# Optimization experiments

Measured on AMD Instinct MI355X. Metric: run time of the kernel, lower is better.

## Reference

```python
import jax, jax.numpy as jnp
import numpy as np

DIM = 64          # out_channels == mamba d_model
D_INNER = 2 * DIM # mamba expand=2
D_STATE = 16
DT_RANK = 4       # ceil(DIM/16)
D_CONV = 4


def setup_inputs() -> dict:
    key = jax.random.key(0)
    ks = jax.random.split(key, 12)
    B, Cin, H, W = 4, 32, 192, 192
    x = jax.random.normal(ks[0], (B, Cin, H, W), jnp.float32)
    conv_w = jax.random.normal(ks[1], (DIM, Cin, 4, 4), jnp.float32) * (1.0 / np.sqrt(Cin * 16))
    conv_b = jnp.zeros((DIM,), jnp.float32)
    ln_g = jnp.ones((DIM,), jnp.float32)
    ln_b = jnp.zeros((DIM,), jnp.float32)
    in_proj_w = jax.random.normal(ks[2], (2 * D_INNER, DIM), jnp.float32) * (1.0 / np.sqrt(DIM))
    conv1d_w = jax.random.normal(ks[3], (D_INNER, 1, D_CONV), jnp.float32) * (1.0 / np.sqrt(D_CONV))
    conv1d_b = jnp.zeros((D_INNER,), jnp.float32)
    x_proj_w = jax.random.normal(ks[4], (DT_RANK + 2 * D_STATE, D_INNER), jnp.float32) * (1.0 / np.sqrt(D_INNER))
    dt_proj_w = jax.random.normal(ks[5], (D_INNER, DT_RANK), jnp.float32) * (DT_RANK ** -0.5)
    dt_proj_b = jnp.log(jnp.expm1(jnp.exp(jax.random.uniform(ks[6], (D_INNER,), jnp.float32,
                jnp.log(1e-3), jnp.log(1e-1)))))  # softplus-inverse of dt in [1e-3,1e-1]
    A_log = jnp.log(jnp.tile(jnp.arange(1, D_STATE + 1, dtype=jnp.float32)[None, :], (D_INNER, 1)))
    D = jnp.ones((D_INNER,), jnp.float32)
    out_proj_w = jax.random.normal(ks[7], (DIM, D_INNER), jnp.float32) * (1.0 / np.sqrt(D_INNER))
    return {"x": x, "conv_w": conv_w, "conv_b": conv_b, "ln_g": ln_g, "ln_b": ln_b,
            "in_proj_w": in_proj_w, "conv1d_w": conv1d_w, "conv1d_b": conv1d_b,
            "x_proj_w": x_proj_w, "dt_proj_w": dt_proj_w, "dt_proj_b": dt_proj_b,
            "A_log": A_log, "D": D, "out_proj_w": out_proj_w}


def _mamba(seq, in_proj_w, conv1d_w, conv1d_b, x_proj_w, dt_proj_w, dt_proj_b, A_log, D, out_proj_w):
    # seq: (B, L, DIM)
    Bb, L, _ = seq.shape
    xz = seq @ in_proj_w.T                          # (B, L, 2*d_inner)
    xm, z = jnp.split(xz, 2, axis=-1)
    # causal depthwise conv1d along L
    xc = jnp.transpose(xm, (0, 2, 1))               # (B, d_inner, L)
    xc = jnp.pad(xc, ((0, 0), (0, 0), (D_CONV - 1, 0)))
    xc = jax.lax.conv_general_dilated(xc, conv1d_w, (1,), 'VALID',
                                      dimension_numbers=('NCH', 'OIH', 'NCH'),
                                      feature_group_count=D_INNER)
    xm = jax.nn.silu(jnp.transpose(xc + conv1d_b[None, :, None], (0, 2, 1)))  # (B, L, d_inner)
    x_dbl = xm @ x_proj_w.T                         # (B, L, dt_rank + 2*d_state)
    dt, Bs, Cs = jnp.split(x_dbl, [DT_RANK, DT_RANK + D_STATE], axis=-1)
    dt = jax.nn.softplus(dt @ dt_proj_w.T + dt_proj_b)  # (B, L, d_inner)
    A = -jnp.exp(A_log)                             # (d_inner, d_state)
    dA = jnp.exp(dt[..., None] * A)                 # (B, L, d_inner, d_state)
    dBx = (dt * xm)[..., None] * Bs[:, :, None, :]  # (B, L, d_inner, d_state)

    def step(h, t):
        dA_t, dBx_t, C_t = t
        h = dA_t * h + dBx_t                        # (B, d_inner, d_state)
        return h, jnp.einsum('bds,bs->bd', h, C_t)

    h0 = jnp.zeros((Bb, D_INNER, D_STATE), seq.dtype)
    _, ys = jax.lax.scan(step, h0, (jnp.swapaxes(dA, 0, 1), jnp.swapaxes(dBx, 0, 1), jnp.swapaxes(Cs, 0, 1)))
    y = jnp.swapaxes(ys, 0, 1) + xm * D             # (B, L, d_inner)
    y = y * jax.nn.silu(z)
    return y @ out_proj_w.T                          # (B, L, DIM)


def reference(x, conv_w, conv_b, ln_g, ln_b, in_proj_w, conv1d_w, conv1d_b,
              x_proj_w, dt_proj_w, dt_proj_b, A_log, D, out_proj_w):
    # ReflectionPad2d(1) + Conv2d(k=4, s=2)
    xp = jnp.pad(x, ((0, 0), (0, 0), (1, 1), (1, 1)), mode='reflect')
    xc = jax.lax.conv_general_dilated(xp, conv_w, (2, 2), 'VALID',
                                      dimension_numbers=('NCHW', 'OIHW', 'NCHW'))
    xc = xc + conv_b[None, :, None, None]           # (B, DIM, H/2, W/2)
    Bb, C, H, W = xc.shape
    seq = jnp.transpose(xc.reshape(Bb, C, H * W), (0, 2, 1))  # (B, L, C)
    mu = seq.mean(-1, keepdims=True)
    var = seq.var(-1, keepdims=True)
    nrm = (seq - mu) * jax.lax.rsqrt(var + 1e-5) * ln_g + ln_b
    out = _mamba(nrm, in_proj_w, conv1d_w, conv1d_b, x_proj_w, dt_proj_w,
                 dt_proj_b, A_log, D, out_proj_w) + seq        # SingleMambaBlock residual
    out = jnp.transpose(out, (0, 2, 1)).reshape(Bb, C, H, W)
    return out + xc                                 # outer residual in Mamba_block.forward
```

## Files before the change

### kernel.cpp

```cpp
#include <hip/hip_runtime.h>
#include <hip/hip_bf16.h>

#define B_   4
#define CIN  32
#define HIN  192
#define WIN  192
#define HO   96
#define WO   96
#define L_   9216
#define C_   64
#define DI   128
#define DS   16
#define NC   256
#define CL   36

typedef unsigned short u16t;
typedef unsigned int   u32t;
typedef short s16x8 __attribute__((ext_vector_type(8)));
typedef float f32x4 __attribute__((ext_vector_type(4)));

__device__ __forceinline__ u16t f2b(float f) {
    u32t u = __float_as_uint(f);
    return (u16t)((u + 0x7fffu + ((u >> 16) & 1u)) >> 16);
}
__device__ __forceinline__ float b2f(u16t h) { return __uint_as_float(((u32t)h) << 16); }
__device__ __forceinline__ void split2(float v, u16t& hi, u16t& lo) {
    hi = f2b(v);
    lo = f2b(v - b2f(hi));
}

#define MFMA16(a, b, c) __builtin_amdgcn_mfma_f32_16x16x32_bf16((a), (b), (c), 0, 0, 0)

__global__ __launch_bounds__(256) void k0_prep(
    const float* __restrict__ ipw, const float* __restrict__ xpw,
    const float* __restrict__ dtw, const float* __restrict__ opw,
    const float* __restrict__ cw,
    u16t* __restrict__ W2p, u16t* __restrict__ Wcp, u16t* __restrict__ W6p,
    u16t* __restrict__ Bp)
{
    int i = blockIdx.x * 256 + threadIdx.x;
    if (i < 32768) {
        int e = i & 7, ln = (i >> 3) & 63, hl = (i >> 9) & 1;
        int nt = (i >> 10) & 15, kt = i >> 14;
        int n = nt * 16 + (ln & 15), k = kt * 32 + (ln >> 4) * 8 + e;
        u16t hi, lo; split2(ipw[n * 64 + k], hi, lo);
        W2p[i] = hl ? lo : hi;
    } else if (i < 32768 + 40960) {
        int j = i - 32768;
        int e = j & 7, ln = (j >> 3) & 63, hl = (j >> 9) & 1;
        int r = j >> 10; int nt = r % 10, kt = r / 10;
        int n = nt * 16 + (ln & 15), k = kt * 32 + (ln >> 4) * 8 + e;
        float v;
        if (n < 128) {
            v = dtw[n * 4 + 0] * xpw[0 * 128 + k] + dtw[n * 4 + 1] * xpw[1 * 128 + k]
              + dtw[n * 4 + 2] * xpw[2 * 128 + k] + dtw[n * 4 + 3] * xpw[3 * 128 + k];
        } else if (n < 144) {
            v = xpw[(4 + n - 128) * 128 + k];
        } else {
            v = xpw[(20 + n - 144) * 128 + k];
        }
        u16t hi, lo; split2(v, hi, lo);
        Wcp[j] = hl ? lo : hi;
    } else if (i < 32768 + 40960 + 16384) {
        int j = i - 32768 - 40960;
        int e = j & 7, ln = (j >> 3) & 63, hl = (j >> 9) & 1;
        int nt = (j >> 10) & 3, kt = j >> 12;
        int n = nt * 16 + (ln & 15), k = kt * 32 + (ln >> 4) * 8 + e;
        u16t hi, lo; split2(opw[n * 128 + k], hi, lo);
        W6p[j] = hl ? lo : hi;
    } else if (i < 32768 + 40960 + 16384 + 32768) {
        int j = i - 32768 - 40960 - 16384;
        int e = j & 7, ln = (j >> 3) & 63, nt = (j >> 9) & 3, kt = j >> 11;
        int n = nt * 16 + (ln & 15), k = kt * 32 + (ln >> 4) * 8 + e;
        Bp[j] = f2b(cw[n * 512 + k]);
    }
}

__global__ __launch_bounds__(256) void k1_conv_ln(
    const float* __restrict__ x, const u16t* __restrict__ Bp,
    const float* __restrict__ cb, const float* __restrict__ g,
    const float* __restrict__ be,
    float* __restrict__ seq, float* __restrict__ nrm)
{
    __shared__ u16t At[64 * 136];
    const int t = threadIdx.x;
    const int pix0 = blockIdx.x * 64;
    const int b = pix0 / L_;
    const int l0 = pix0 % L_;
    const int wave = t >> 6, ln = t & 63;
    const int quad = ln >> 4, col = ln & 15;

    const int kk = t & 127;
    const int m0 = t >> 7;
    const int kh = (kk >> 2) & 3, kw = kk & 3, cil = kk >> 4;

    f32x4 acc[4];
    #pragma unroll
    for (int nt = 0; nt < 4; ++nt) acc[nt] = (f32x4){0.f, 0.f, 0.f, 0.f};

    const u16t* arow = &At[(wave * 16 + col) * 136 + quad * 8];

    for (int cc = 0; cc < 4; ++cc) {
        __syncthreads();
        const float* xb = x + (b * CIN + cc * 8 + cil) * (HIN * WIN);
        #pragma unroll 4
        for (int j = 0; j < 32; ++j) {
            int m = m0 + 2 * j;
            int l = l0 + m;
            int oh = l / WO, ow = l - oh * WO;
            int ih = 2 * oh + kh - 1; ih = ih < 0 ? 1 : (ih >= HIN ? 2 * HIN - 2 - ih : ih);
            int iw = 2 * ow + kw - 1; iw = iw < 0 ? 1 : (iw >= WIN ? 2 * WIN - 2 - iw : iw);
            At[m * 136 + kk] = f2b(xb[ih * WIN + iw]);
        }
        __syncthreads();

        #pragma unroll
        for (int ktl = 0; ktl < 4; ++ktl) {
            s16x8 a = *reinterpret_cast<const s16x8*>(arow + ktl * 32);
            const u16t* bpb = Bp + (cc * 4 + ktl) * 2048 + ln * 8;
            #pragma unroll
            for (int nt = 0; nt < 4; ++nt) {
                s16x8 bf = *reinterpret_cast<const s16x8*>(bpb + nt * 512);
                acc[nt] = MFMA16(a, bf, acc[nt]);
            }
        }
    }

    float gv[4], bv[4], cbv[4];
    #pragma unroll
    for (int nt = 0; nt < 4; ++nt) {
        gv[nt] = g[nt * 16 + col];
        bv[nt] = be[nt * 16 + col];
        cbv[nt] = cb[nt * 16 + col];
    }
    #pragma unroll
    for (int r = 0; r < 4; ++r) {
        float v0 = acc[0][r] + cbv[0];
        float v1 = acc[1][r] + cbv[1];
        float v2 = acc[2][r] + cbv[2];
        float v3 = acc[3][r] + cbv[3];
        float s1 = (v0 + v1) + (v2 + v3);
        float s2 = (v0 * v0 + v1 * v1) + (v2 * v2 + v3 * v3);
        #pragma unroll
        for (int mk = 1; mk <= 8; mk <<= 1) {
            s1 += __shfl_xor(s1, mk);
            s2 += __shfl_xor(s2, mk);
        }
        float mu = s1 * (1.0f / 64.0f);
        float var = s2 * (1.0f / 64.0f) - mu * mu;
        float rs = rsqrtf(var + 1e-5f);
        int pix = pix0 + wave * 16 + quad * 4 + r;
        float* sp = seq + pix * 64 + col;
        float* np = nrm + pix * 64 + col;
        sp[0]  = v0; sp[16] = v1; sp[32] = v2; sp[48] = v3;
        np[0]  = (v0 - mu) * rs * gv[0] + bv[0];
        np[16] = (v1 - mu) * rs * gv[1] + bv[1];
        np[32] = (v2 - mu) * rs * gv[2] + bv[2];
        np[48] = (v3 - mu) * rs * gv[3] + bv[3];
    }
}

__global__ __launch_bounds__(256) void g2_inproj(
    const float* __restrict__ nrm, const u16t* __restrict__ W2p,
    float* __restrict__ xm, float* __restrict__ sz)
{
    __shared__ u16t Ah[64 * 72], Al[64 * 72];
    const int t = threadIdx.x;
    const int row0 = blockIdx.x * 64;

    for (int idx = t; idx < 1024; idx += 256) {
        int r = idx >> 4, kq = (idx & 15) * 4;
        float4 v = *reinterpret_cast<const float4*>(nrm + (row0 + r) * 64 + kq);
        u16t h, l;
        split2(v.x, h, l); Ah[r * 72 + kq + 0] = h; Al[r * 72 + kq + 0] = l;
        split2(v.y, h, l); Ah[r * 72 + kq + 1] = h; Al[r * 72 + kq + 1] = l;
        split2(v.z, h, l); Ah[r * 72 + kq + 2] = h; Al[r * 72 + kq + 2] = l;
        split2(v.w, h, l); Ah[r * 72 + kq + 3] = h; Al[r * 72 + kq + 3] = l;
    }
    __syncthreads();

    const int wave = t >> 6, ln = t & 63, quad = ln >> 4, col = ln & 15;
    f32x4 acc[16];
    #pragma unroll
    for (int nt = 0; nt < 16; ++nt) acc[nt] = (f32x4){0.f, 0.f, 0.f, 0.f};

    const int abase = (wave * 16 + col) * 72 + quad * 8;
    #pragma unroll
    for (int kt = 0; kt < 2; ++kt) {
        s16x8 ah = *reinterpret_cast<const s16x8*>(Ah + abase + kt * 32);
        s16x8 al = *reinterpret_cast<const s16x8*>(Al + abase + kt * 32);
        const u16t* bb = W2p + (kt * 16) * 1024 + ln * 8;
        #pragma unroll
        for (int nt = 0; nt < 16; ++nt) {
            s16x8 bh = *reinterpret_cast<const s16x8*>(bb + nt * 1024);
            s16x8 bl = *reinterpret_cast<const s16x8*>(bb + nt * 1024 + 512);
            acc[nt] = MFMA16(al, bh, acc[nt]);
            acc[nt] = MFMA16(ah, bl, acc[nt]);
            acc[nt] = MFMA16(ah, bh, acc[nt]);
        }
    }

    const int mrow = row0 + wave * 16 + quad * 4;
    #pragma unroll
    for (int nt = 0; nt < 16; ++nt) {
        int n = nt * 16 + col;
        #pragma unroll
        for (int r = 0; r < 4; ++r) {
            float v = acc[nt][r];
            if (n < 128) {
                xm[(mrow + r) * DI + n] = v;
            } else {
                sz[(mrow + r) * DI + (n - 128)] = v / (1.f + __expf(-v));
            }
        }
    }
}

__global__ __launch_bounds__(256) void k3_dwconv(
    const float* __restrict__ xm, const float* __restrict__ w,
    const float* __restrict__ bia, float* __restrict__ u)
{
    const int gid = blockIdx.x * 256 + threadIdx.x;
    const int c = gid & 127;
    const int g = gid >> 7;
    const int bl0 = g * 4;
    const int l0 = bl0 % L_;

    float w0 = w[c * 4 + 0], w1 = w[c * 4 + 1];
    float w2 = w[c * 4 + 2], w3 = w[c * 4 + 3];
    float bv = bia[c];

    float xv[7];
    if (l0 == 0) { xv[0] = xv[1] = xv[2] = 0.f; }
    else {
        xv[0] = xm[(bl0 - 3) * DI + c];
        xv[1] = xm[(bl0 - 2) * DI + c];
        xv[2] = xm[(bl0 - 1) * DI + c];
    }
    #pragma unroll
    for (int j = 0; j < 4; ++j) xv[3 + j] = xm[(bl0 + j) * DI + c];

    #pragma unroll
    for (int j = 0; j < 4; ++j) {
        float a = bv + xv[j] * w0 + xv[j + 1] * w1 + xv[j + 2] * w2 + xv[j + 3] * w3;
        u[(bl0 + j) * DI + c] = a / (1.f + __expf(-a));
    }
}

__global__ __launch_bounds__(256) void g4_xproj(
    const float* __restrict__ u, const u16t* __restrict__ Wcp,
    const float* __restrict__ dtb,
    float* __restrict__ dt, float* __restrict__ Bs, float* __restrict__ Cs)
{
    __shared__ u16t Ah[64 * 136], Al[64 * 136];
    const int t = threadIdx.x;
    const int row0 = blockIdx.x * 64;

    for (int idx = t; idx < 2048; idx += 256) {
        int r = idx >> 5, kq = (idx & 31) * 4;
        float4 v = *reinterpret_cast<const float4*>(u + (row0 + r) * DI + kq);
        u16t h, l;
        split2(v.x, h, l); Ah[r * 136 + kq + 0] = h; Al[r * 136 + kq + 0] = l;
        split2(v.y, h, l); Ah[r * 136 + kq + 1] = h; Al[r * 136 + kq + 1] = l;
        split2(v.z, h, l); Ah[r * 136 + kq + 2] = h; Al[r * 136 + kq + 2] = l;
        split2(v.w, h, l); Ah[r * 136 + kq + 3] = h; Al[r * 136 + kq + 3] = l;
    }
    __syncthreads();

    const int wave = t >> 6, ln = t & 63, quad = ln >> 4, col = ln & 15;
    f32x4 acc[10];
    #pragma unroll
    for (int nt = 0; nt < 10; ++nt) acc[nt] = (f32x4){0.f, 0.f, 0.f, 0.f};

    const int abase = (wave * 16 + col) * 136 + quad * 8;
    #pragma unroll
    for (int kt = 0; kt < 4; ++kt) {
        s16x8 ah = *reinterpret_cast<const s16x8*>(Ah + abase + kt * 32);
        s16x8 al = *reinterpret_cast<const s16x8*>(Al + abase + kt * 32);
        const u16t* bb = Wcp + (kt * 10) * 1024 + ln * 8;
        #pragma unroll
        for (int nt = 0; nt < 10; ++nt) {
            s16x8 bh = *reinterpret_cast<const s16x8*>(bb + nt * 1024);
            s16x8 bl = *reinterpret_cast<const s16x8*>(bb + nt * 1024 + 512);
            acc[nt] = MFMA16(al, bh, acc[nt]);
            acc[nt] = MFMA16(ah, bl, acc[nt]);
            acc[nt] = MFMA16(ah, bh, acc[nt]);
        }
    }

    const int mrow = row0 + wave * 16 + quad * 4;
    #pragma unroll
    for (int nt = 0; nt < 8; ++nt) {
        int n = nt * 16 + col;
        float db = dtb[n];
        #pragma unroll
        for (int r = 0; r < 4; ++r) {
            float v = acc[nt][r] + db;
            v = v > 20.f ? v : log1pf(__expf(v));
            dt[(mrow + r) * DI + n] = v;
        }
    }
    #pragma unroll
    for (int r = 0; r < 4; ++r) {
        Bs[(mrow + r) * DS + col] = acc[8][r];
        Cs[(mrow + r) * DS + col] = acc[9][r];
    }
}

__global__ __launch_bounds__(128) void k5a(
    const float* __restrict__ dt, const float* __restrict__ u,
    const float* __restrict__ Bsb, const float* __restrict__ alog,
    float* __restrict__ P, float* __restrict__ HP)
{
    const int bk = blockIdx.x;
    const int b = bk / NC, k = bk - b * NC;
    const int c = threadIdx.x;
    float As[DS];
    #pragma unroll
    for (int s = 0; s < DS; ++s) As[s] = -__expf(alog[c * DS + s]);
    float Pp[DS], hp[DS];
    #pragma unroll
    for (int s = 0; s < DS; ++s) { Pp[s] = 1.f; hp[s] = 0.f; }

    const int l0 = k * CL;
    for (int i = 0; i < CL; ++i) {
        const int row = b * L_ + l0 + i;
        float dtv = dt[row * DI + c];
        float uv = u[row * DI + c];
        float dtu = dtv * uv;
        const float4* Bq = reinterpret_cast<const float4*>(Bsb + row * DS);
        float Bv[DS];
        #pragma unroll
        for (int q = 0; q < 4; ++q)
            *reinterpret_cast<float4*>(&Bv[q * 4]) = Bq[q];
        #pragma unroll
        for (int s = 0; s < DS; ++s) {
            float dA = __expf(dtv * As[s]);
            hp[s] = dA * hp[s] + dtu * Bv[s];
            Pp[s] *= dA;
        }
    }
    float* Pd = P + bk * 2048 + c * DS;
    float* Hd = HP + bk * 2048 + c * DS;
    #pragma unroll
    for (int q = 0; q < 4; ++q) {
        reinterpret_cast<float4*>(Pd)[q] = *reinterpret_cast<float4*>(&Pp[q * 4]);
        reinterpret_cast<float4*>(Hd)[q] = *reinterpret_cast<float4*>(&hp[q * 4]);
    }
}

__global__ __launch_bounds__(64) void k5b(
    float* __restrict__ P, const float* __restrict__ HP)
{
    const int t = blockIdx.x * 64 + threadIdx.x;
    const int b = t >> 11, cs = t & 2047;
    float carry = 0.f;
    for (int k = 0; k < NC; ++k) {
        const int idx = (b * NC + k) * 2048 + cs;
        float p = P[idx];
        float hp = HP[idx];
        P[idx] = carry;
        carry = hp + p * carry;
    }
}

__global__ __launch_bounds__(128) void k5c_out(
    const float* __restrict__ dt, const float* __restrict__ u,
    const float* __restrict__ Bsb, const float* __restrict__ Csb,
    const float* __restrict__ sz, const float* __restrict__ alog,
    const float* __restrict__ Db, const float* __restrict__ HI,
    const float* __restrict__ seq, const u16t* __restrict__ W6p,
    float* __restrict__ out)
{
    __shared__ u16t Yh[64 * 136], Yl[64 * 136];
    const int bk = blockIdx.x;
    const int b = bk / NC, k = bk - b * NC;
    const int c = threadIdx.x;
    float As[DS];
    #pragma unroll
    for (int s = 0; s < DS; ++s) As[s] = -__expf(alog[c * DS + s]);
    const float Dc = Db[c];
    float h[DS];
    const float* Hs = HI + bk * 2048 + c * DS;
    #pragma unroll
    for (int q = 0; q < 4; ++q)
        *reinterpret_cast<float4*>(&h[q * 4]) = reinterpret_cast<const float4*>(Hs)[q];

    const int l0 = k * CL;
    for (int i = 0; i < CL; ++i) {
        const int row = b * L_ + l0 + i;
        float dtv = dt[row * DI + c];
        float uv = u[row * DI + c];
        float szv = sz[row * DI + c];
        float dtu = dtv * uv;
        const float4* Bq = reinterpret_cast<const float4*>(Bsb + row * DS);
        const float4* Cq = reinterpret_cast<const float4*>(Csb + row * DS);
        float Bv[DS], Cv[DS];
        #pragma unroll
        for (int q = 0; q < 4; ++q) {
            *reinterpret_cast<float4*>(&Bv[q * 4]) = Bq[q];
            *reinterpret_cast<float4*>(&Cv[q * 4]) = Cq[q];
        }
        float ya[4] = {0.f, 0.f, 0.f, 0.f};
        #pragma unroll
        for (int s = 0; s < DS; ++s) {
            float dA = __expf(dtv * As[s]);
            h[s] = dA * h[s] + dtu * Bv[s];
            ya[s & 3] += h[s] * Cv[s];
        }
        float yv = ((ya[0] + ya[1]) + (ya[2] + ya[3]) + uv * Dc) * szv;
        u16t hi, lo; split2(yv, hi, lo);
        Yh[i * 136 + c] = hi;
        Yl[i * 136 + c] = lo;
    }
    __syncthreads();

    const int wave = c >> 6, ln = c & 63, quad = ln >> 4, col = ln & 15;
    f32x4 acc[2][4];
    #pragma unroll
    for (int mt = 0; mt < 2; ++mt)
        #pragma unroll
        for (int nt = 0; nt < 4; ++nt) acc[mt][nt] = (f32x4){0.f, 0.f, 0.f, 0.f};

    #pragma unroll
    for (int mt = 0; mt < 2; ++mt) {
        const int m = (wave * 2 + mt) * 16 + col;
        const int abase = m * 136 + quad * 8;
        #pragma unroll
        for (int kt = 0; kt < 4; ++kt) {
            s16x8 ah = (m < CL + 16) ? *reinterpret_cast<const s16x8*>(Yh + abase + kt * 32)
                                     : (s16x8){0,0,0,0,0,0,0,0};
            s16x8 al = (m < CL + 16) ? *reinterpret_cast<const s16x8*>(Yl + abase + kt * 32)
                                     : (s16x8){0,0,0,0,0,0,0,0};
            const u16t* bb = W6p + (kt * 4) * 1024 + ln * 8;
            #pragma unroll
            for (int nt = 0; nt < 4; ++nt) {
                s16x8 bh = *reinterpret_cast<const s16x8*>(bb + nt * 1024);
                s16x8 bl = *reinterpret_cast<const s16x8*>(bb + nt * 1024 + 512);
                acc[mt][nt] = MFMA16(al, bh, acc[mt][nt]);
                acc[mt][nt] = MFMA16(ah, bl, acc[mt][nt]);
                acc[mt][nt] = MFMA16(ah, bh, acc[mt][nt]);
            }
        }
    }
    __syncthreads();

    float* oT = reinterpret_cast<float*>(Yh);
    #pragma unroll
    for (int mt = 0; mt < 2; ++mt) {
        const int mb = (wave * 2 + mt) * 16 + quad * 4;
        #pragma unroll
        for (int nt = 0; nt < 4; ++nt) {
            const int n = nt * 16 + col;
            #pragma unroll
            for (int r = 0; r < 4; ++r) {
                const int m = mb + r;
                if (m < CL)
                    oT[n * 37 + m] = acc[mt][nt][r]
                                   + 2.f * seq[(b * L_ + l0 + m) * 64 + n];
            }
        }
    }
    __syncthreads();

    for (int i = 0; i < 18; ++i) {
        int idx = i * 128 + c;
        int n = idx / CL, l = idx - n * CL;
        out[(b * 64 + n) * L_ + l0 + l] = oT[n * 37 + l];
    }
}

extern "C" void kernel_launch(void* const* d_in, const int* in_sizes, int n_in,
                              void* d_out, int out_size, void* d_ws, size_t ws_size,
                              hipStream_t stream)
{
    const float* x    = (const float*)d_in[0];
    const float* cw   = (const float*)d_in[1];
    const float* cb   = (const float*)d_in[2];
    const float* g    = (const float*)d_in[3];
    const float* be   = (const float*)d_in[4];
    const float* ipw  = (const float*)d_in[5];
    const float* c1w  = (const float*)d_in[6];
    const float* c1b  = (const float*)d_in[7];
    const float* xpw  = (const float*)d_in[8];
    const float* dtw  = (const float*)d_in[9];
    const float* dtb  = (const float*)d_in[10];
    const float* alog = (const float*)d_in[11];
    const float* Db   = (const float*)d_in[12];
    const float* opw  = (const float*)d_in[13];

    float* ws  = (float*)d_ws;
    float* seq = ws;
    float* nrm = seq + 2359296;
    float* xm  = nrm + 2359296;
    float* sz  = xm + 4718592;
    float* u   = sz + 4718592;
    float* dt  = u + 4718592;
    u16t*  W2p = (u16t*)(dt + 4718592);
    u16t*  Wcp = W2p + 32768;
    u16t*  W6p = Wcp + 40960;
    u16t*  Bp  = W6p + 16384;
    float* Bs  = nrm;
    float* Cs  = nrm + 589824;
    float* P   = xm;
    float* HP  = xm + 2097152;

    k0_prep   <<<480, 256, 0, stream>>>(ipw, xpw, dtw, opw, cw, W2p, Wcp, W6p, Bp);
    k1_conv_ln<<<576, 256, 0, stream>>>(x, Bp, cb, g, be, seq, nrm);
    g2_inproj <<<576, 256, 0, stream>>>(nrm, W2p, xm, sz);
    k3_dwconv <<<4608, 256, 0, stream>>>(xm, c1w, c1b, u);
    g4_xproj  <<<576, 256, 0, stream>>>(u, Wcp, dtb, dt, Bs, Cs);
    k5a       <<<B_ * NC, 128, 0, stream>>>(dt, u, Bs, alog, P, HP);
    k5b      <<<128, 64, 0, stream>>>(P, HP);
    k5c_out   <<<B_ * NC, 128, 0, stream>>>(dt, u, Bs, Cs, sz, alog, Db, P,
                                            seq, W6p, (float*)d_out);
}
```

Baseline: 260.2 us.

## Fuse causal depthwise conv1d and SiLU into x-proj and scan kernels

Removes the separate depthwise-conv kernel and its u buffer; the conv+SiLU is recomputed from xm inside g4_xproj (reading 4 neighbouring rows per element) and inside both scan kernels using a rolling 3-value window. P/HP get their own workspace since xm must stay live. This trades a kernel launch and an 18MB write plus reads of u for redundant conv arithmetic and extra xm reads in three kernels.

```diff
diff --git a/kernel.cpp b/kernel.cpp
--- a/kernel.cpp
+++ b/kernel.cpp
@@ -216,54 +216,48 @@
     }
 }
 
-__global__ __launch_bounds__(256) void k3_dwconv(
-    const float* __restrict__ xm, const float* __restrict__ w,
-    const float* __restrict__ bia, float* __restrict__ u)
-{
-    const int gid = blockIdx.x * 256 + threadIdx.x;
-    const int c = gid & 127;
-    const int g = gid >> 7;
-    const int bl0 = g * 4;
-    const int l0 = bl0 % L_;
-
-    float w0 = w[c * 4 + 0], w1 = w[c * 4 + 1];
-    float w2 = w[c * 4 + 2], w3 = w[c * 4 + 3];
-    float bv = bia[c];
-
-    float xv[7];
-    if (l0 == 0) { xv[0] = xv[1] = xv[2] = 0.f; }
-    else {
-        xv[0] = xm[(bl0 - 3) * DI + c];
-        xv[1] = xm[(bl0 - 2) * DI + c];
-        xv[2] = xm[(bl0 - 1) * DI + c];
-    }
-    #pragma unroll
-    for (int j = 0; j < 4; ++j) xv[3 + j] = xm[(bl0 + j) * DI + c];
-
-    #pragma unroll
-    for (int j = 0; j < 4; ++j) {
-        float a = bv + xv[j] * w0 + xv[j + 1] * w1 + xv[j + 2] * w2 + xv[j + 3] * w3;
-        u[(bl0 + j) * DI + c] = a / (1.f + __expf(-a));
-    }
-}
-
 __global__ __launch_bounds__(256) void g4_xproj(
-    const float* __restrict__ u, const u16t* __restrict__ Wcp,
+    const float* __restrict__ xm, const u16t* __restrict__ Wcp,
+    const float* __restrict__ c1w, const float* __restrict__ c1b,
     const float* __restrict__ dtb,
     float* __restrict__ dt, float* __restrict__ Bs, float* __restrict__ Cs)
 {
     __shared__ u16t Ah[64 * 136], Al[64 * 136];
     const int t = threadIdx.x;
     const int row0 = blockIdx.x * 64;
+    const int l0g = row0 % L_;
 
     for (int idx = t; idx < 2048; idx += 256) {
         int r = idx >> 5, kq = (idx & 31) * 4;
-        float4 v = *reinterpret_cast<const float4*>(u + (row0 + r) * DI + kq);
+        int grow = row0 + r;
+        int lr = l0g + r;
+        float4 xv[4];
+        #pragma unroll
+        for (int j = 0; j < 4; ++j) {
+            if (lr - 3 + j >= 0)
+                xv[j] = *reinterpret_cast<const float4*>(xm + (grow - 3 + j) * DI + kq);
+            else
+                xv[j] = (float4){0.f, 0.f, 0.f, 0.f};
+        }
+        float4 b4 = *reinterpret_cast<const float4*>(c1b + kq);
+        float4 t0 = *reinterpret_cast<const float4*>(c1w + (kq + 0) * 4);
+        float4 t1 = *reinterpret_cast<const float4*>(c1w + (kq + 1) * 4);
+        float4 t2 = *reinterpret_cast<const float4*>(c1w + (kq + 2) * 4);
+        float4 t3 = *reinterpret_cast<const float4*>(c1w + (kq + 3) * 4);
+        float4 a;
+        a.x = b4.x + t0.x * xv[0].x + t0.y * xv[1].x + t0.z * xv[2].x + t0.w * xv[3].x;
+        a.y = b4.y + t1.x * xv[0].y + t1.y * xv[1].y + t1.z * xv[2].y + t1.w * xv[3].y;
+        a.z = b4.z + t2.x * xv[0].z + t2.y * xv[1].z + t2.z * xv[2].z + t2.w * xv[3].z;
+        a.w = b4.w + t3.x * xv[0].w + t3.y * xv[1].w + t3.z * xv[2].w + t3.w * xv[3].w;
+        a.x = a.x / (1.f + __expf(-a.x));
+        a.y = a.y / (1.f + __expf(-a.y));
+        a.z = a.z / (1.f + __expf(-a.z));
+        a.w = a.w / (1.f + __expf(-a.w));
         u16t h, l;
-        split2(v.x, h, l); Ah[r * 136 + kq + 0] = h; Al[r * 136 + kq + 0] = l;
-        split2(v.y, h, l); Ah[r * 136 + kq + 1] = h; Al[r * 136 + kq + 1] = l;
-        split2(v.z, h, l); Ah[r * 136 + kq + 2] = h; Al[r * 136 + kq + 2] = l;
-        split2(v.w, h, l); Ah[r * 136 + kq + 3] = h; Al[r * 136 + kq + 3] = l;
+        split2(a.x, h, l); Ah[r * 136 + kq + 0] = h; Al[r * 136 + kq + 0] = l;
+        split2(a.y, h, l); Ah[r * 136 + kq + 1] = h; Al[r * 136 + kq + 1] = l;
+        split2(a.z, h, l); Ah[r * 136 + kq + 2] = h; Al[r * 136 + kq + 2] = l;
+        split2(a.w, h, l); Ah[r * 136 + kq + 3] = h; Al[r * 136 + kq + 3] = l;
     }
     __syncthreads();
 
@@ -308,8 +302,9 @@
 }
 
 __global__ __launch_bounds__(128) void k5a(
-    const float* __restrict__ dt, const float* __restrict__ u,
+    const float* __restrict__ dt, const float* __restrict__ xm,
     const float* __restrict__ Bsb, const float* __restrict__ alog,
+    const float* __restrict__ c1w, const float* __restrict__ c1b,
     float* __restrict__ P, float* __restrict__ HP)
 {
     const int bk = blockIdx.x;
@@ -318,15 +313,31 @@
     float As[DS];
     #pragma unroll
     for (int s = 0; s < DS; ++s) As[s] = -__expf(alog[c * DS + s]);
+    const float w0 = c1w[c * 4 + 0], w1 = c1w[c * 4 + 1];
+    const float w2 = c1w[c * 4 + 2], w3 = c1w[c * 4 + 3];
+    const float cb1 = c1b[c];
+
+    const int l0 = k * CL;
+    const int row0 = b * L_ + l0;
+    float x0, x1, x2;
+    if (k == 0) { x0 = x1 = x2 = 0.f; }
+    else {
+        x0 = xm[(row0 - 3) * DI + c];
+        x1 = xm[(row0 - 2) * DI + c];
+        x2 = xm[(row0 - 1) * DI + c];
+    }
+
     float Pp[DS], hp[DS];
     #pragma unroll
     for (int s = 0; s < DS; ++s) { Pp[s] = 1.f; hp[s] = 0.f; }
 
-    const int l0 = k * CL;
     for (int i = 0; i < CL; ++i) {
-        const int row = b * L_ + l0 + i;
+        const int row = row0 + i;
         float dtv = dt[row * DI + c];
-        float uv = u[row * DI + c];
+        float x3 = xm[row * DI + c];
+        float a = cb1 + x0 * w0 + x1 * w1 + x2 * w2 + x3 * w3;
+        float uv = a / (1.f + __expf(-a));
+        x0 = x1; x1 = x2; x2 = x3;
         float dtu = dtv * uv;
         const float4* Bq = reinterpret_cast<const float4*>(Bsb + row * DS);
         float Bv[DS];
@@ -365,11 +376,12 @@
 }
 
 __global__ __launch_bounds__(128) void k5c_out(
-    const float* __restrict__ dt, const float* __restrict__ u,
+    const float* __restrict__ dt, const float* __restrict__ xm,
     const float* __restrict__ Bsb, const float* __restrict__ Csb,
     const float* __restrict__ sz, const float* __restrict__ alog,
     const float* __restrict__ Db, const float* __restrict__ HI,
     const float* __restrict__ seq, const u16t* __restrict__ W6p,
+    const float* __restrict__ c1w, const float* __restrict__ c1b,
     float* __restrict__ out)
 {
     __shared__ u16t Yh[64 * 136], Yl[64 * 136];
@@ -380,6 +392,9 @@
     #pragma unroll
     for (int s = 0; s < DS; ++s) As[s] = -__expf(alog[c * DS + s]);
     const float Dc = Db[c];
+    const float w0 = c1w[c * 4 + 0], w1 = c1w[c * 4 + 1];
+    const float w2 = c1w[c * 4 + 2], w3 = c1w[c * 4 + 3];
+    const float cb1 = c1b[c];
     float h[DS];
     const float* Hs = HI + bk * 2048 + c * DS;
     #pragma unroll
@@ -387,11 +402,23 @@
         *reinterpret_cast<float4*>(&h[q * 4]) = reinterpret_cast<const float4*>(Hs)[q];
 
     const int l0 = k * CL;
+    const int row0 = b * L_ + l0;
+    float x0, x1, x2;
+    if (k == 0) { x0 = x1 = x2 = 0.f; }
+    else {
+        x0 = xm[(row0 - 3) * DI + c];
+        x1 = xm[(row0 - 2) * DI + c];
+        x2 = xm[(row0 - 1) * DI + c];
+    }
+
     for (int i = 0; i < CL; ++i) {
-        const int row = b * L_ + l0 + i;
+        const int row = row0 + i;
         float dtv = dt[row * DI + c];
-        float uv = u[row * DI + c];
+        float x3 = xm[row * DI + c];
         float szv = sz[row * DI + c];
+        float a = cb1 + x0 * w0 + x1 * w1 + x2 * w2 + x3 * w3;
+        float uv = a / (1.f + __expf(-a));
+        x0 = x1; x1 = x2; x2 = x3;
         float dtu = dtv * uv;
         const float4* Bq = reinterpret_cast<const float4*>(Bsb + row * DS);
         const float4* Cq = reinterpret_cast<const float4*>(Csb + row * DS);
@@ -494,24 +521,22 @@
     float* nrm = seq + 2359296;
     float* xm  = nrm + 2359296;
     float* sz  = xm + 4718592;
-    float* u   = sz + 4718592;
-    float* dt  = u + 4718592;
-    u16t*  W2p = (u16t*)(dt + 4718592);
+    float* dt  = sz + 4718592;
+    float* P   = dt + 4718592;
+    float* HP  = P + 2097152;
+    u16t*  W2p = (u16t*)(HP + 2097152);
     u16t*  Wcp = W2p + 32768;
     u16t*  W6p = Wcp + 40960;
     u16t*  Bp  = W6p + 16384;
     float* Bs  = nrm;
     float* Cs  = nrm + 589824;
-    float* P   = xm;
-    float* HP  = xm + 2097152;
 
     k0_prep   <<<480, 256, 0, stream>>>(ipw, xpw, dtw, opw, cw, W2p, Wcp, W6p, Bp);
     k1_conv_ln<<<576, 256, 0, stream>>>(x, Bp, cb, g, be, seq, nrm);
     g2_inproj <<<576, 256, 0, stream>>>(nrm, W2p, xm, sz);
-    k3_dwconv <<<4608, 256, 0, stream>>>(xm, c1w, c1b, u);
-    g4_xproj  <<<576, 256, 0, stream>>>(u, Wcp, dtb, dt, Bs, Cs);
-    k5a       <<<B_ * NC, 128, 0, stream>>>(dt, u, Bs, alog, P, HP);
+    g4_xproj  <<<576, 256, 0, stream>>>(xm, Wcp, c1w, c1b, dtb, dt, Bs, Cs);
+    k5a       <<<B_ * NC, 128, 0, stream>>>(dt, xm, Bs, alog, c1w, c1b, P, HP);
     k5b      <<<128, 64, 0, stream>>>(P, HP);
-    k5c_out   <<<B_ * NC, 128, 0, stream>>>(dt, u, Bs, Cs, sz, alog, Db, P,
-                                            seq, W6p, (float*)d_out);
-}
+    k5c_out   <<<B_ * NC, 128, 0, stream>>>(dt, xm, Bs, Cs, sz, alog, Db, P,
+                                            seq, W6p, c1w, c1b, (float*)d_out);
+}
```

Measured after the change: 258.6 us. Within noise of the previous version (-0.6%).
